# Kernel optimization log

Measured on AMD Instinct MI355X. Metric: run time of the kernel, lower is better.

Reference implementation:

```python
import jax, jax.numpy as jnp
import numpy as np

DEPTH = 3
NUM_MOLS = 2000
ATOMS_PER_MOL = 50
NA = NUM_MOLS * ATOMS_PER_MOL + 1   # +1 chemprop zero-padding row
NB = 2 * NUM_MOLS * ATOMS_PER_MOL + 1
MAX_NB = 6
ATOM_FDIM, BOND_FDIM, H = 133, 147, 300


def setup_inputs() -> dict:
    key = jax.random.key(0)
    ks = jax.random.split(key, 12)
    f_atoms = jax.random.normal(ks[0], (NA, ATOM_FDIM), jnp.float32)
    f_bonds = jax.random.normal(ks[1], (NB, BOND_FDIM), jnp.float32)
    # zero padding row (index 0) as in chemprop BatchMolGraph
    f_atoms = f_atoms.at[0].set(0.0)
    f_bonds = f_bonds.at[0].set(0.0)
    w_atoms = jax.random.uniform(ks[2], (NA,), jnp.float32, 0.5, 1.0)
    w_bonds = jax.random.uniform(ks[3], (NB,), jnp.float32, 0.5, 1.0)
    degree_of_polym = jax.random.uniform(ks[4], (NUM_MOLS,), jnp.float32, 0.5, 1.5)
    W_i = jax.random.normal(ks[5], (BOND_FDIM, H), jnp.float32) / np.sqrt(BOND_FDIM)
    W_h = jax.random.normal(ks[6], (H, H), jnp.float32) / np.sqrt(H)
    W_o = jax.random.normal(ks[7], (ATOM_FDIM + H, H), jnp.float32) / np.sqrt(ATOM_FDIM + H)
    b_o = jax.random.normal(ks[8], (H,), jnp.float32) * 0.01
    a2b = jax.random.randint(ks[9], (NA, MAX_NB), 0, NB, jnp.int32)
    b2a = jax.random.randint(ks[10], (NB,), 0, NA, jnp.int32)
    b2revb = jax.random.randint(ks[11], (NB,), 0, NB, jnp.int32)
    # segment id per real atom (padding row 0 excluded), contiguous molecules
    mol_index = (jnp.arange(NA - 1, dtype=jnp.int32) // ATOMS_PER_MOL)
    return dict(f_atoms=f_atoms, f_bonds=f_bonds, w_atoms=w_atoms, w_bonds=w_bonds,
                degree_of_polym=degree_of_polym, W_i=W_i, W_h=W_h, W_o=W_o, b_o=b_o,
                a2b=a2b, b2a=b2a, b2revb=b2revb, mol_index=mol_index)


def reference(f_atoms, f_bonds, w_atoms, w_bonds, degree_of_polym,
              W_i, W_h, W_o, b_o, a2b, b2a, b2revb, mol_index):
    # bond-message D-MPNN (atom_messages=False, undirected=False, relu, no dropout)
    inp = f_bonds @ W_i                       # [NB, H]
    message = jax.nn.relu(inp)
    w_nei = w_bonds[a2b]                      # [NA, MAX_NB]
    for _ in range(DEPTH - 1):
        nei = message[a2b] * w_nei[..., None] # [NA, MAX_NB, H] weighted gather
        a_message = nei.sum(axis=1)           # [NA, H]
        message = a_message[b2a] - message[b2revb] * w_bonds[:, None]
        message = jax.nn.relu(inp + message @ W_h)
    # final atom readout
    a_message = (message[a2b] * w_nei[..., None]).sum(axis=1)   # [NA, H]
    a_input = jnp.concatenate([f_atoms, a_message], axis=1)     # [NA, ATOM_FDIM+H]
    atom_hiddens = jax.nn.relu(a_input @ W_o + b_o)
    # per-molecule weighted mean over real atoms (row 0 is padding)
    h = atom_hiddens[1:] * w_atoms[1:, None]
    num_mols = degree_of_polym.shape[0]
    mol_sum = jax.ops.segment_sum(h, mol_index, num_segments=num_mols)
    w_sum = jax.ops.segment_sum(w_atoms[1:], mol_index, num_segments=num_mols)
    mol_vecs = degree_of_polym[:, None] * (mol_sum / w_sum[:, None])
    return mol_vecs
```

## Files before the change

### kernel.cpp

```cpp
#include <hip/hip_runtime.h>

typedef __bf16 bf16;
typedef bf16 bf16x8 __attribute__((ext_vector_type(8)));
typedef float f32x4 __attribute__((ext_vector_type(4)));

#define NUM_MOLS 2000
#define APM 50
#define NA (NUM_MOLS*APM+1)
#define NB (2*NUM_MOLS*APM+1)
#define MAX_NB 6
#define AF 133
#define BFD 147
#define H 300
#define HP 320
#define KIP 192
#define KO 448
#define AOFF 136
#define BM 64
#define BKT 64
#define LDT 72

__global__ void k_prep_wi(const float* __restrict__ Wi, bf16* __restrict__ Wt){
    int i = blockIdx.x*256 + threadIdx.x; if (i >= HP*KIP) return;
    int n = i / KIP, k = i % KIP;
    float v = (k < BFD && n < H) ? Wi[k*H + n] : 0.f;
    Wt[i] = (bf16)v;
}
__global__ void k_prep_wh(const float* __restrict__ Wh, bf16* __restrict__ Wt){
    int i = blockIdx.x*256 + threadIdx.x; if (i >= HP*HP) return;
    int n = i / HP, k = i % HP;
    float v = (k < H && n < H) ? Wh[k*H + n] : 0.f;
    Wt[i] = (bf16)v;
}
__global__ void k_prep_wo(const float* __restrict__ Wo, bf16* __restrict__ Wt){
    int i = blockIdx.x*256 + threadIdx.x; if (i >= HP*KO) return;
    int n = i / KO, k = i % KO;
    float v = 0.f;
    if (n < H) {
        if (k < AF)                       v = Wo[k*H + n];
        else if (k >= AOFF && k < AOFF+H) v = Wo[(k - AOFF + AF)*H + n];
    }
    Wt[i] = (bf16)v;
}
__global__ void k_init_cat(const float* __restrict__ fa, bf16* __restrict__ cat){
    long u = (long)blockIdx.x*256 + threadIdx.x; if (u >= (long)NA*18) return;
    int c = (int)(u % 18); long a = u / 18;
    bf16x8 v;
    if (c < 17) {
        int c0 = c*8;
        #pragma unroll
        for (int j=0;j<8;j++){
            int col = c0 + j;
            float f = (col < AF) ? fa[a*AF + col] : 0.f;
            v[j] = (bf16)f;
        }
        *(bf16x8*)(cat + a*KO + c0) = v;
    } else {
        #pragma unroll
        for (int j=0;j<8;j++) v[j] = (bf16)0.f;
        *(bf16x8*)(cat + a*KO + 440) = v;
    }
}

__global__ void k_gather_amsg(const bf16* __restrict__ msg, const int* __restrict__ a2b,
                              const float* __restrict__ w_bonds,
                              bf16* __restrict__ out, int out_stride, int col_off, int nchunks){
    long u = (long)blockIdx.x*256 + threadIdx.x;
    if (u >= (long)NA*nchunks) return;
    int c = (int)(u % nchunks); long a = u / nchunks;
    int c0 = c*8;
    float acc[8] = {0,0,0,0,0,0,0,0};
    #pragma unroll
    for (int k=0;k<MAX_NB;k++){
        int b = a2b[a*MAX_NB + k];
        float w = w_bonds[b];
        bf16x8 m = *(const bf16x8*)(msg + (long)b*HP + c0);
        #pragma unroll
        for (int j=0;j<8;j++) acc[j] += w * fmaxf((float)m[j], 0.f);
    }
    bf16x8 o;
    #pragma unroll
    for (int j=0;j<8;j++) o[j] = (bf16)acc[j];
    *(bf16x8*)(out + (long)a*out_stride + col_off + c0) = o;
}

template<int MODE>
__global__ __launch_bounds__(512, 4)
void k_gemm(const void* __restrict__ Asrc, const bf16* __restrict__ msgsrc,
            const int* __restrict__ b2a, const int* __restrict__ b2revb,
            const float* __restrict__ w_bonds,
            const bf16* __restrict__ Bt, int K, int M,
            const bf16* __restrict__ add, const float* __restrict__ bias,
            bf16* __restrict__ out)
{
    __shared__ bf16 As[BM][LDT];
    __shared__ bf16 Bs[HP][LDT];
    int t = threadIdx.x;
    int row0 = blockIdx.x * BM;
    int wave = t >> 6, lane = t & 63;
    int wm = wave >> 2, wn = wave & 3;
    int kr = lane >> 4, lr = lane & 15;
    f32x4 acc[2][5] = {};

    int sr = t >> 3;
    int sc = (t & 7) * 8;
    int arow = row0 + sr; if (arow >= M) arow = M - 1;
    int ia = 0, ir = 0; float w = 0.f;
    if (MODE == 1) { ia = b2a[arow]; ir = b2revb[arow]; w = w_bonds[arow]; }

    for (int k0 = 0; k0 < K; k0 += BKT) {
        bf16x8 av;
        if (MODE == 0) {
            const float* fb = (const float*)Asrc;
            #pragma unroll
            for (int j = 0; j < 8; j++) {
                int k = k0 + sc + j;
                av[j] = (bf16)(k < BFD ? fb[(long)arow*BFD + k] : 0.f);
            }
        } else if (MODE == 1) {
            const bf16* am = (const bf16*)Asrc;
            bf16x8 a8 = *(const bf16x8*)(am     + (long)ia*HP + k0 + sc);
            bf16x8 m8 = *(const bf16x8*)(msgsrc + (long)ir*HP + k0 + sc);
            #pragma unroll
            for (int j = 0; j < 8; j++)
                av[j] = (bf16)((float)a8[j] - fmaxf((float)m8[j], 0.f) * w);
        } else {
            av = *(const bf16x8*)((const bf16*)Asrc + (long)arow*KO + k0 + sc);
        }
        bf16x8 bv[5];
        #pragma unroll
        for (int i = 0; i < 5; i++) {
            int c = t + 512*i;
            int br = c >> 3, bc = (c & 7) * 8;
            bv[i] = *(const bf16x8*)(Bt + (long)br*K + k0 + bc);
        }
        __syncthreads();
        *(bf16x8*)(&As[sr][sc]) = av;
        #pragma unroll
        for (int i = 0; i < 5; i++) {
            int c = t + 512*i;
            int br = c >> 3, bc = (c & 7) * 8;
            *(bf16x8*)(&Bs[br][bc]) = bv[i];
        }
        __syncthreads();
        #pragma unroll
        for (int kk = 0; kk < BKT; kk += 32) {
            bf16x8 af[2], bfr[5];
            #pragma unroll
            for (int m = 0; m < 2; m++)
                af[m] = *(const bf16x8*)(&As[wm*32 + m*16 + lr][kk + kr*8]);
            #pragma unroll
            for (int n = 0; n < 5; n++)
                bfr[n] = *(const bf16x8*)(&Bs[wn*80 + n*16 + lr][kk + kr*8]);
            #pragma unroll
            for (int m = 0; m < 2; m++)
                #pragma unroll
                for (int n = 0; n < 5; n++)
                    acc[m][n] = __builtin_amdgcn_mfma_f32_16x16x32_bf16(af[m], bfr[n], acc[m][n], 0, 0, 0);
        }
    }
    #pragma unroll
    for (int m = 0; m < 2; m++)
    #pragma unroll
    for (int n = 0; n < 5; n++)
    #pragma unroll
    for (int r = 0; r < 4; r++) {
        int row = row0 + wm*32 + m*16 + kr*4 + r;
        if (row >= M) continue;
        int col = wn*80 + n*16 + lr;
        float v = acc[m][n][r];
        if (add)  v += (float)add[(long)row*HP + col];
        if (bias) v += (col < H) ? bias[col] : 0.f;
        if (MODE == 2) v = fmaxf(v, 0.f);
        out[(long)row*HP + col] = (bf16)v;
    }
}

__global__ void k_seg(const bf16* __restrict__ ah, const float* __restrict__ w_atoms,
                      const float* __restrict__ dop, float* __restrict__ out){
    int m = blockIdx.x; int t = threadIdx.x;
    __shared__ float ws_sum;
    float w = 0.f;
    if (t < APM) w = w_atoms[1 + m*APM + t];
    if (t < 64) {
        for (int o=32;o;o>>=1) w += __shfl_down(w, o);
        if (t==0) ws_sum = w;
    }
    __syncthreads();
    float scale = dop[m] / ws_sum;
    for (int h = t; h < H; h += 256) {
        float acc = 0.f;
        for (int j=0;j<APM;j++){
            int a = 1 + m*APM + j;
            acc += (float)ah[(long)a*HP + h] * w_atoms[a];
        }
        out[m*H + h] = acc * scale;
    }
}

__global__ void k_zero(float* __restrict__ out, int n){
    int i = blockIdx.x*256 + threadIdx.x;
    if (i < n) out[i] = 0.f;
}

extern "C" void kernel_launch(void* const* d_in, const int* in_sizes, int n_in,
                              void* d_out, int out_size, void* d_ws, size_t ws_size,
                              hipStream_t stream) {
    const float* f_atoms = (const float*)d_in[0];
    const float* f_bonds = (const float*)d_in[1];
    const float* w_atoms = (const float*)d_in[2];
    const float* w_bonds = (const float*)d_in[3];
    const float* dop     = (const float*)d_in[4];
    const float* W_i     = (const float*)d_in[5];
    const float* W_h     = (const float*)d_in[6];
    const float* W_o     = (const float*)d_in[7];
    const float* b_o     = (const float*)d_in[8];
    const int*   a2b     = (const int*)d_in[9];
    const int*   b2a     = (const int*)d_in[10];
    const int*   b2revb  = (const int*)d_in[11];
    float* out = (float*)d_out;
    (void)in_sizes; (void)n_in;

    const size_t R_BIG = ((size_t)NB*HP*2 + 255) & ~(size_t)255;
    const size_t R_ATM = ((size_t)NA*HP*2 + 255) & ~(size_t)255;
    const size_t R_WI  = ((size_t)HP*KIP*2 + 255) & ~(size_t)255;
    const size_t R_WH  = ((size_t)HP*HP*2 + 255) & ~(size_t)255;
    const size_t R_WO  = ((size_t)HP*KO*2 + 255) & ~(size_t)255;
    const size_t need  = 3*R_BIG + R_ATM + R_WI + R_WH + R_WO;

    if (ws_size < need) {
        k_zero<<<(out_size+255)/256, 256, 0, stream>>>(out, out_size);
        return;
    }

    char* ws = (char*)d_ws;
    bf16* inp  = (bf16*)ws;
    bf16* msgA = (bf16*)(ws + R_BIG);
    bf16* msgB = (bf16*)(ws + 2*R_BIG);
    bf16* amsg = (bf16*)(ws + 3*R_BIG);
    bf16* wit  = (bf16*)(ws + 3*R_BIG + R_ATM);
    bf16* wht  = (bf16*)((char*)wit + R_WI);
    bf16* wot  = (bf16*)((char*)wht + R_WH);
    bf16* cat  = msgA;
    bf16* ah   = amsg;

    k_prep_wi<<<(HP*KIP+255)/256, 256, 0, stream>>>(W_i, wit);
    k_prep_wh<<<(HP*HP+255)/256, 256, 0, stream>>>(W_h, wht);
    k_prep_wo<<<(HP*KO+255)/256, 256, 0, stream>>>(W_o, wot);

    const int GB = (NB + BM - 1) / BM;
    const int GA = (NA + BM - 1) / BM;

    k_gemm<0><<<GB, 512, 0, stream>>>(f_bonds, nullptr, nullptr, nullptr, nullptr,
                                      wit, KIP, NB, nullptr, nullptr, inp);
    k_gather_amsg<<<(int)(((long)NA*40+255)/256), 256, 0, stream>>>(
        inp, a2b, w_bonds, amsg, HP, 0, 40);
    k_gemm<1><<<GB, 512, 0, stream>>>(amsg, inp, b2a, b2revb, w_bonds,
                                      wht, HP, NB, inp, nullptr, msgA);
    k_gather_amsg<<<(int)(((long)NA*40+255)/256), 256, 0, stream>>>(
        msgA, a2b, w_bonds, amsg, HP, 0, 40);
    k_gemm<1><<<GB, 512, 0, stream>>>(amsg, msgA, b2a, b2revb, w_bonds,
                                      wht, HP, NB, inp, nullptr, msgB);
    k_init_cat<<<(int)(((long)NA*18+255)/256), 256, 0, stream>>>(f_atoms, cat);
    k_gather_amsg<<<(int)(((long)NA*38+255)/256), 256, 0, stream>>>(
        msgB, a2b, w_bonds, cat, KO, AOFF, 38);
    k_gemm<2><<<GA, 512, 0, stream>>>(cat, nullptr, nullptr, nullptr, nullptr,
                                      wot, KO, NA, nullptr, b_o, ah);
    k_seg<<<NUM_MOLS, 256, 0, stream>>>(ah, w_atoms, dop, out);
}
```

Measured before the change: 833.6 us.

## Stage full-K A tile in LDS once and read weights directly from global

The GEMM kernel now loads the whole K extent of the A tile into shared memory in a single pass, followed by one barrier, replacing the per-64-wide K loop with its two barriers per step. B fragments (the transposed weights) are read straight from global memory/L2 into registers instead of being staged through LDS, which frees the large Bs buffer. K becomes a template parameter so the K loop fully unrolls. The trade-off is redundant global weight reads across waves and blocks, a larger A tile footprint in LDS for big K, and the loss of the min-blocks occupancy hint.

```diff
diff --git a/kernel.cpp b/kernel.cpp
--- a/kernel.cpp
+++ b/kernel.cpp
@@ -17,8 +17,6 @@
 #define KO 448
 #define AOFF 136
 #define BM 64
-#define BKT 64
-#define LDT 72
 
 __global__ void k_prep_wi(const float* __restrict__ Wi, bf16* __restrict__ Wt){
     int i = blockIdx.x*256 + threadIdx.x; if (i >= HP*KIP) return;
@@ -84,81 +82,87 @@
     *(bf16x8*)(out + (long)a*out_stride + col_off + c0) = o;
 }
 
-template<int MODE>
-__global__ __launch_bounds__(512, 4)
+template<int MODE, int K>
+__global__ __launch_bounds__(512)
 void k_gemm(const void* __restrict__ Asrc, const bf16* __restrict__ msgsrc,
             const int* __restrict__ b2a, const int* __restrict__ b2revb,
             const float* __restrict__ w_bonds,
-            const bf16* __restrict__ Bt, int K, int M,
+            const bf16* __restrict__ Bt, int M,
             const bf16* __restrict__ add, const float* __restrict__ bias,
             bf16* __restrict__ out)
 {
-    __shared__ bf16 As[BM][LDT];
-    __shared__ bf16 Bs[HP][LDT];
-    int t = threadIdx.x;
-    int row0 = blockIdx.x * BM;
-    int wave = t >> 6, lane = t & 63;
-    int wm = wave >> 2, wn = wave & 3;
-    int kr = lane >> 4, lr = lane & 15;
+    constexpr int LDTE = K + 24;
+    __shared__ bf16 As[BM * LDTE];
+    const int t = threadIdx.x;
+    const int row0 = blockIdx.x * BM;
+
+    const int sr = t >> 3;
+    const int c8 = (t & 7) * 8;
+    int arow = row0 + sr; if (arow >= M) arow = M - 1;
+    constexpr int NJ = K / 64;
+
+    if (MODE == 0) {
+        const float* fb = (const float*)Asrc;
+        #pragma unroll
+        for (int j = 0; j < NJ; j++) {
+            int col = c8 + j*64;
+            bf16x8 av;
+            #pragma unroll
+            for (int jj = 0; jj < 8; jj++) {
+                int k = col + jj;
+                av[jj] = (bf16)(k < BFD ? fb[(long)arow*BFD + k] : 0.f);
+            }
+            *(bf16x8*)(&As[sr*LDTE + col]) = av;
+        }
+    } else if (MODE == 1) {
+        const bf16* am = (const bf16*)Asrc;
+        const int ia = b2a[arow], ir = b2revb[arow];
+        const float w = w_bonds[arow];
+        bf16x8 a8[NJ], m8[NJ];
+        #pragma unroll
+        for (int j = 0; j < NJ; j++) {
+            a8[j] = *(const bf16x8*)(am     + (long)ia*HP + c8 + j*64);
+            m8[j] = *(const bf16x8*)(msgsrc + (long)ir*HP + c8 + j*64);
+        }
+        #pragma unroll
+        for (int j = 0; j < NJ; j++) {
+            bf16x8 av;
+            #pragma unroll
+            for (int jj = 0; jj < 8; jj++)
+                av[jj] = (bf16)((float)a8[j][jj] - fmaxf((float)m8[j][jj], 0.f) * w);
+            *(bf16x8*)(&As[sr*LDTE + c8 + j*64]) = av;
+        }
+    } else {
+        const bf16* am = (const bf16*)Asrc;
+        #pragma unroll
+        for (int j = 0; j < NJ; j++) {
+            bf16x8 av = *(const bf16x8*)(am + (long)arow*KO + c8 + j*64);
+            *(bf16x8*)(&As[sr*LDTE + c8 + j*64]) = av;
+        }
+    }
+    __syncthreads();
+
+    const int wave = t >> 6, lane = t & 63;
+    const int wm = wave >> 2, wn = wave & 3;
+    const int kr = lane >> 4, lr = lane & 15;
     f32x4 acc[2][5] = {};
 
-    int sr = t >> 3;
-    int sc = (t & 7) * 8;
-    int arow = row0 + sr; if (arow >= M) arow = M - 1;
-    int ia = 0, ir = 0; float w = 0.f;
-    if (MODE == 1) { ia = b2a[arow]; ir = b2revb[arow]; w = w_bonds[arow]; }
-
-    for (int k0 = 0; k0 < K; k0 += BKT) {
-        bf16x8 av;
-        if (MODE == 0) {
-            const float* fb = (const float*)Asrc;
-            #pragma unroll
-            for (int j = 0; j < 8; j++) {
-                int k = k0 + sc + j;
-                av[j] = (bf16)(k < BFD ? fb[(long)arow*BFD + k] : 0.f);
-            }
-        } else if (MODE == 1) {
-            const bf16* am = (const bf16*)Asrc;
-            bf16x8 a8 = *(const bf16x8*)(am     + (long)ia*HP + k0 + sc);
-            bf16x8 m8 = *(const bf16x8*)(msgsrc + (long)ir*HP + k0 + sc);
-            #pragma unroll
-            for (int j = 0; j < 8; j++)
-                av[j] = (bf16)((float)a8[j] - fmaxf((float)m8[j], 0.f) * w);
-        } else {
-            av = *(const bf16x8*)((const bf16*)Asrc + (long)arow*KO + k0 + sc);
-        }
-        bf16x8 bv[5];
-        #pragma unroll
-        for (int i = 0; i < 5; i++) {
-            int c = t + 512*i;
-            int br = c >> 3, bc = (c & 7) * 8;
-            bv[i] = *(const bf16x8*)(Bt + (long)br*K + k0 + bc);
-        }
-        __syncthreads();
-        *(bf16x8*)(&As[sr][sc]) = av;
-        #pragma unroll
-        for (int i = 0; i < 5; i++) {
-            int c = t + 512*i;
-            int br = c >> 3, bc = (c & 7) * 8;
-            *(bf16x8*)(&Bs[br][bc]) = bv[i];
-        }
-        __syncthreads();
-        #pragma unroll
-        for (int kk = 0; kk < BKT; kk += 32) {
-            bf16x8 af[2], bfr[5];
-            #pragma unroll
-            for (int m = 0; m < 2; m++)
-                af[m] = *(const bf16x8*)(&As[wm*32 + m*16 + lr][kk + kr*8]);
+    #pragma unroll
+    for (int kk = 0; kk < K; kk += 32) {
+        bf16x8 af[2], bfr[5];
+        #pragma unroll
+        for (int m = 0; m < 2; m++)
+            af[m] = *(const bf16x8*)(&As[(wm*32 + m*16 + lr)*LDTE + kk + kr*8]);
+        #pragma unroll
+        for (int n = 0; n < 5; n++)
+            bfr[n] = *(const bf16x8*)(Bt + (long)(wn*80 + n*16 + lr)*K + kk + kr*8);
+        #pragma unroll
+        for (int m = 0; m < 2; m++)
             #pragma unroll
             for (int n = 0; n < 5; n++)
-                bfr[n] = *(const bf16x8*)(&Bs[wn*80 + n*16 + lr][kk + kr*8]);
-            #pragma unroll
-            for (int m = 0; m < 2; m++)
-                #pragma unroll
-                for (int n = 0; n < 5; n++)
-                    acc[m][n] = __builtin_amdgcn_mfma_f32_16x16x32_bf16(af[m], bfr[n], acc[m][n], 0, 0, 0);
-        }
-    }
+                acc[m][n] = __builtin_amdgcn_mfma_f32_16x16x32_bf16(af[m], bfr[n], acc[m][n], 0, 0, 0);
+    }
+
     #pragma unroll
     for (int m = 0; m < 2; m++)
     #pragma unroll
@@ -251,20 +255,20 @@
     const int GB = (NB + BM - 1) / BM;
     const int GA = (NA + BM - 1) / BM;
 
-    k_gemm<0><<<GB, 512, 0, stream>>>(f_bonds, nullptr, nullptr, nullptr, nullptr,
-                                      wit, KIP, NB, nullptr, nullptr, inp);
+    k_gemm<0, KIP><<<GB, 512, 0, stream>>>(f_bonds, nullptr, nullptr, nullptr, nullptr,
+                                           wit, NB, nullptr, nullptr, inp);
     k_gather_amsg<<<(int)(((long)NA*40+255)/256), 256, 0, stream>>>(
         inp, a2b, w_bonds, amsg, HP, 0, 40);
-    k_gemm<1><<<GB, 512, 0, stream>>>(amsg, inp, b2a, b2revb, w_bonds,
-                                      wht, HP, NB, inp, nullptr, msgA);
+    k_gemm<1, HP><<<GB, 512, 0, stream>>>(amsg, inp, b2a, b2revb, w_bonds,
+                                          wht, NB, inp, nullptr, msgA);
     k_gather_amsg<<<(int)(((long)NA*40+255)/256), 256, 0, stream>>>(
         msgA, a2b, w_bonds, amsg, HP, 0, 40);
-    k_gemm<1><<<GB, 512, 0, stream>>>(amsg, msgA, b2a, b2revb, w_bonds,
-                                      wht, HP, NB, inp, nullptr, msgB);
+    k_gemm<1, HP><<<GB, 512, 0, stream>>>(amsg, msgA, b2a, b2revb, w_bonds,
+                                          wht, NB, inp, nullptr, msgB);
     k_init_cat<<<(int)(((long)NA*18+255)/256), 256, 0, stream>>>(f_atoms, cat);
     k_gather_amsg<<<(int)(((long)NA*38+255)/256), 256, 0, stream>>>(
         msgB, a2b, w_bonds, cat, KO, AOFF, 38);
-    k_gemm<2><<<GA, 512, 0, stream>>>(cat, nullptr, nullptr, nullptr, nullptr,
-                                      wot, KO, NA, nullptr, b_o, ah);
+    k_gemm<2, KO><<<GA, 512, 0, stream>>>(cat, nullptr, nullptr, nullptr, nullptr,
+                                          wot, NA, nullptr, b_o, ah);
     k_seg<<<NUM_MOLS, 256, 0, stream>>>(ah, w_atoms, dop, out);
 }
```

After: 1.074 ms. +28.8%, slower.
